# Performance work log

Measured on AMD Instinct MI355X. Metric: run time of the kernel, lower is better.

Reference implementation:

```python
import jax, jax.numpy as jnp
import numpy as np

B, L, D, E, R, NMOD = 8, 2048, 4096, 4, 8, 7

def setup_inputs() -> dict:
    key = jax.random.key(0)
    ks = jax.random.split(key, 8)
    return {
        "x": jax.random.normal(ks[0], (B, L, D), dtype=jnp.float32) * 0.02,
        "expert_scores": jax.random.uniform(ks[1], (B, E), dtype=jnp.float32),
        "W_base": jax.random.normal(ks[2], (D, D), dtype=jnp.float32) * 0.02,
        "b_base": jnp.zeros((D,), dtype=jnp.float32),
        "gating_W": jax.random.normal(ks[3], (D, D), dtype=jnp.float32) * 0.02,
        "W_r": jax.random.normal(ks[4], (NMOD, D), dtype=jnp.float32) * 0.02,
        "lora_A": jax.random.normal(ks[5], (E, R, D), dtype=jnp.float32) * 0.02,
        "lora_B": jax.random.normal(ks[6], (E, D, R), dtype=jnp.float32) * 0.02,
        "module_idx": 0,
        "k": 2,
    }

def _gate_weights(expert_scores, module_prob, k, dtype):
    # rank experts by their random score (descending); Top-K -> weight 1/K
    order = jnp.argsort(-expert_scores, axis=-1)           # [B, E]
    rank = jnp.argsort(order, axis=-1)                     # [B, E] rank of each expert
    k_lo = max(1, k // 2)
    w_hi = (rank < k).astype(dtype) / k                    # prob > 0.5 branch
    w_lo = (rank < k_lo).astype(dtype) / k_lo              # prob <= 0.5 branch
    return jnp.where((module_prob > 0.5)[:, None], w_hi, w_lo)  # [B, E]

def reference(x, expert_scores, W_base, b_base, gating_W, W_r, lora_A, lora_B, module_idx, k):
    # Pooler: last token representation
    pooled = x[:, -1, :]                                   # [B, D]
    # Router: softmax(g(h) W_r) -> per-module probability
    gated = pooled @ gating_W.T                            # [B, D]
    logits = gated @ W_r.T                                 # [B, NMOD]
    probs = jax.nn.softmax(logits, axis=-1)
    module_prob = probs[:, module_idx]                     # [B]
    gate = _gate_weights(expert_scores, module_prob, k, x.dtype)  # [B, E]
    # Base linear projection
    base = x @ W_base.T + b_base                           # [B, L, D]
    # LoRA experts: sum_e gate[b,e] * (x @ A_e^T) @ B_e^T
    t = jnp.einsum('bli,eri->belr', x, lora_A)             # [B, E, L, R]
    lora = jnp.einsum('belr,eor,be->blo', t, lora_B, gate) # [B, L, D]
    return base + lora
```

## Files before the change

kernel.cpp:

```cpp
#include <hip/hip_runtime.h>
#include <hip/hip_bf16.h>


typedef short short8 __attribute__((ext_vector_type(8)));
typedef float f32x4v __attribute__((ext_vector_type(4)));

#define M_DIM 16384
#define N_DIM 4096
#define K_DIM 4160
#define D_DIM 4096
#define NGRP 130

__device__ __forceinline__ unsigned short f2b(float f) {
  unsigned u = __builtin_bit_cast(unsigned, f);
  return (unsigned short)((u + 0x7FFFu + ((u >> 16) & 1u)) >> 16);
}
__device__ __forceinline__ void async_copy16(void* lds, const void* g) {
  __builtin_amdgcn_global_load_lds(
      (const __attribute__((address_space(1))) void*)g,
      (__attribute__((address_space(3))) void*)lds, 16, 0, 0);
}
__device__ __forceinline__ short8 frag_ld(const short* base, int row, int ks, int hi, int lo) {
  return *(const short8*)(&base[row * 64 + (((ks * 4 + hi) ^ (lo & 7)) * 8)]);
}

__global__ __launch_bounds__(256) void cvt_x_k(const float* __restrict__ x,
                                               short* __restrict__ xa) {
  size_t idx = (size_t)blockIdx.x * 256 + threadIdx.x;
  size_t row = idx / 520;
  int cc = (int)(idx % 520);
  short8 o;
  if (cc < 512) {
    const float* src = x + row * (size_t)D_DIM + (size_t)cc * 8;
    float4 a = *(const float4*)(src);
    float4 b = *(const float4*)(src + 4);
    o[0] = (short)f2b(a.x); o[1] = (short)f2b(a.y);
    o[2] = (short)f2b(a.z); o[3] = (short)f2b(a.w);
    o[4] = (short)f2b(b.x); o[5] = (short)f2b(b.y);
    o[6] = (short)f2b(b.z); o[7] = (short)f2b(b.w);
  } else {
#pragma unroll
    for (int t = 0; t < 8; ++t) o[t] = 0;
  }
  *(short8*)(xa + row * (size_t)K_DIM + (size_t)cc * 8) = o;
}

__global__ __launch_bounds__(256) void cvt_w_la_k(const float* __restrict__ Wb,
                                                  const float* __restrict__ lB,
                                                  const float* __restrict__ lA,
                                                  short* __restrict__ wa,
                                                  short* __restrict__ lAb) {
  if (blockIdx.x < 8320) {
    size_t idx = (size_t)blockIdx.x * 256 + threadIdx.x;
    size_t row = idx / 520;
    int cc = (int)(idx % 520);
    short8 o;
    if (cc < 512) {
      const float* src = Wb + row * (size_t)D_DIM + (size_t)cc * 8;
      float4 a = *(const float4*)(src);
      float4 b = *(const float4*)(src + 4);
      o[0] = (short)f2b(a.x); o[1] = (short)f2b(a.y);
      o[2] = (short)f2b(a.z); o[3] = (short)f2b(a.w);
      o[4] = (short)f2b(b.x); o[5] = (short)f2b(b.y);
      o[6] = (short)f2b(b.z); o[7] = (short)f2b(b.w);
    } else if (cc < 516) {
      int e = cc - 512;
      const float* src = lB + (size_t)e * (D_DIM * 8) + row * 8;
      float4 a = *(const float4*)(src);
      float4 b = *(const float4*)(src + 4);
      o[0] = (short)f2b(a.x); o[1] = (short)f2b(a.y);
      o[2] = (short)f2b(a.z); o[3] = (short)f2b(a.w);
      o[4] = (short)f2b(b.x); o[5] = (short)f2b(b.y);
      o[6] = (short)f2b(b.z); o[7] = (short)f2b(b.w);
    } else {
#pragma unroll
      for (int t = 0; t < 8; ++t) o[t] = 0;
    }
    *(short8*)(wa + row * (size_t)K_DIM + (size_t)cc * 8) = o;
  } else {
    size_t i = (size_t)(blockIdx.x - 8320) * 256 + threadIdx.x;
    const float* s = lA + i * 8;
    float4 a = *(const float4*)s;
    float4 b = *(const float4*)(s + 4);
    short8 o;
    o[0] = (short)f2b(a.x); o[1] = (short)f2b(a.y);
    o[2] = (short)f2b(a.z); o[3] = (short)f2b(a.w);
    o[4] = (short)f2b(b.x); o[5] = (short)f2b(b.y);
    o[6] = (short)f2b(b.z); o[7] = (short)f2b(b.w);
    *(short8*)(lAb + i * 8) = o;
  }
}

__global__ __launch_bounds__(256) void gated_k(const float* __restrict__ x,
                                               const float* __restrict__ gW,
                                               float* __restrict__ gated) {
  const int j = blockIdx.x;
  const int tid = threadIdx.x;
  float acc[8];
#pragma unroll
  for (int b = 0; b < 8; ++b) acc[b] = 0.f;
  const float* w = gW + (size_t)j * D_DIM;
  for (int i = tid * 4; i < D_DIM; i += 1024) {
    float4 wv = *(const float4*)(w + i);
#pragma unroll
    for (int b = 0; b < 8; ++b) {
      const float* p = x + ((size_t)b * 2048 + 2047) * D_DIM + i;
      float4 pv = *(const float4*)p;
      acc[b] += wv.x * pv.x + wv.y * pv.y + wv.z * pv.z + wv.w * pv.w;
    }
  }
  __shared__ float red[8][4];
  const int lane = tid & 63, wv_ = tid >> 6;
#pragma unroll
  for (int b = 0; b < 8; ++b) {
    float v = acc[b];
    v += __shfl_down(v, 32); v += __shfl_down(v, 16); v += __shfl_down(v, 8);
    v += __shfl_down(v, 4);  v += __shfl_down(v, 2);  v += __shfl_down(v, 1);
    if (lane == 0) red[b][wv_] = v;
  }
  __syncthreads();
  if (tid < 8)
    gated[(size_t)tid * D_DIM + j] = red[tid][0] + red[tid][1] + red[tid][2] + red[tid][3];
}

__global__ void gate_k(const float* __restrict__ gated, const float* __restrict__ Wr,
                       const float* __restrict__ scores, const int* __restrict__ midx_p,
                       const int* __restrict__ kp, float* __restrict__ gate) {
  const int lane = threadIdx.x;
  float acc[56];
#pragma unroll
  for (int t = 0; t < 56; ++t) acc[t] = 0.f;
  for (int i = lane * 4; i < D_DIM; i += 256) {
    float4 g[8]; float4 w[7];
#pragma unroll
    for (int b = 0; b < 8; ++b) g[b] = *(const float4*)(gated + (size_t)b * D_DIM + i);
#pragma unroll
    for (int m = 0; m < 7; ++m) w[m] = *(const float4*)(Wr + (size_t)m * D_DIM + i);
#pragma unroll
    for (int m = 0; m < 7; ++m)
#pragma unroll
      for (int b = 0; b < 8; ++b)
        acc[m * 8 + b] += w[m].x * g[b].x + w[m].y * g[b].y + w[m].z * g[b].z + w[m].w * g[b].w;
  }
  __shared__ float Ls[56];
#pragma unroll
  for (int t = 0; t < 56; ++t) {
    float v = acc[t];
    v += __shfl_xor(v, 1); v += __shfl_xor(v, 2); v += __shfl_xor(v, 4);
    v += __shfl_xor(v, 8); v += __shfl_xor(v, 16); v += __shfl_xor(v, 32);
    if (lane == t) Ls[t] = v;
  }
  __syncthreads();
  if (lane < 8) {
    const int b = lane;
    float mx = -1e30f;
    for (int m = 0; m < 7; ++m) mx = fmaxf(mx, Ls[m * 8 + b]);
    float s = 0.f;
    for (int m = 0; m < 7; ++m) s += expf(Ls[m * 8 + b] - mx);
    const int mi = midx_p[0];
    const float mp = expf(Ls[mi * 8 + b] - mx) / s;
    int kv = kp[0]; if (kv < 1) kv = 1;
    int klo = kv >> 1; if (klo < 1) klo = 1;
    float sc[4];
#pragma unroll
    for (int e = 0; e < 4; ++e) sc[e] = scores[b * 4 + e];
#pragma unroll
    for (int e = 0; e < 4; ++e) {
      int rank = 0;
#pragma unroll
      for (int e2 = 0; e2 < 4; ++e2)
        rank += (sc[e2] > sc[e] || (sc[e2] == sc[e] && e2 < e)) ? 1 : 0;
      float wv = (mp > 0.5f) ? ((rank < kv) ? 1.0f / (float)kv : 0.f)
                             : ((rank < klo) ? 1.0f / (float)klo : 0.f);
      gate[b * 4 + e] = wv;
    }
  }
}

__global__ __launch_bounds__(256) void lora_t_k(const short* __restrict__ XA,
                                                const short* __restrict__ LAb,
                                                const float* __restrict__ gate,
                                                short* __restrict__ xa_w) {
  __shared__ short As[4096];
  __shared__ short Bs[2048];
  const int tid = threadIdx.x, lane = tid & 63, wave = tid >> 6;
  const int lo = lane & 15, hi = lane >> 4;
  const size_t row0 = (size_t)blockIdx.x * 64;
  const int srow = tid >> 3;
  const int slot = (tid & 7) ^ (srow & 7);
  const short* gA = XA + (row0 + srow) * (size_t)K_DIM + slot * 8;
  const short* gB = LAb + (size_t)srow * D_DIM + slot * 8;
  f32x4v acc[2] = {};

  for (int t = 0; t < 64; ++t) {
    const int kt = t * 64;
    char* la = (char*)As + wave * 1024;
    char* lb = (char*)Bs + wave * 1024;
    async_copy16(la, gA + kt);
    async_copy16(la + 4096, gA + (size_t)32 * K_DIM + kt);
    async_copy16(lb, gB + kt);
    __syncthreads();
    short8 a0 = frag_ld(As, wave * 16 + lo, 0, hi, lo);
    short8 a1 = frag_ld(As, wave * 16 + lo, 1, hi, lo);
    short8 b00 = frag_ld(Bs, lo, 0, hi, lo);
    short8 b01 = frag_ld(Bs, lo, 1, hi, lo);
    short8 b10 = frag_ld(Bs, 16 + lo, 0, hi, lo);
    short8 b11 = frag_ld(Bs, 16 + lo, 1, hi, lo);
    acc[0] = __builtin_amdgcn_mfma_f32_16x16x32_bf16(a0, b00, acc[0], 0, 0, 0);
    acc[0] = __builtin_amdgcn_mfma_f32_16x16x32_bf16(a1, b01, acc[0], 0, 0, 0);
    acc[1] = __builtin_amdgcn_mfma_f32_16x16x32_bf16(a0, b10, acc[1], 0, 0, 0);
    acc[1] = __builtin_amdgcn_mfma_f32_16x16x32_bf16(a1, b11, acc[1], 0, 0, 0);
    __syncthreads();
  }
  const int b = (int)(row0 >> 11);
#pragma unroll
  for (int ni = 0; ni < 2; ++ni) {
    const int col = ni * 16 + lo;
    const float g = gate[b * 4 + (col >> 3)];
#pragma unroll
    for (int j = 0; j < 4; ++j) {
      const size_t r = row0 + wave * 16 + hi * 4 + j;
      xa_w[r * (size_t)K_DIM + 4096 + col] = (short)f2b(acc[ni][j] * g);
    }
  }
}

__global__ __launch_bounds__(512, 2) void gemm_k(const short* __restrict__ A,
                                                 const short* __restrict__ B,
                                                 const float* __restrict__ bias,
                                                 float* __restrict__ C) {
  __shared__ short As[5][8192];
  __shared__ short Bs[5][8192];
  const int tid = threadIdx.x;
  const int lane = tid & 63;
  const int wave = tid >> 6;
  const int wm = wave >> 2;
  const int wn = wave & 3;
  const int lo = lane & 15, hi = lane >> 4;

  const int wg = (blockIdx.x & 7) * 128 + (blockIdx.x >> 3);
  const int brow = wg >> 4;
  const int bcol = wg & 15;

  const int srow = tid >> 2;
  const int schunk = (tid & 3) ^ ((tid >> 3) & 3);
  const short* srcA = A + (size_t)(brow * 256 + srow) * K_DIM + schunk * 8;
  const short* srcB = B + (size_t)(bcol * 256 + srow) * K_DIM + schunk * 8;
  char* ldsA0 = (char*)(&As[0][0]) + wave * 1024;
  char* ldsB0 = (char*)(&Bs[0][0]) + wave * 1024;

  const int csw = (hi ^ ((lo >> 1) & 3)) * 8;
  const int aro = (wm * 128 + lo) * 32 + csw;
  const int bro = (wn * 64 + lo) * 32 + csw;

  float bz[4];
#pragma unroll
  for (int ni = 0; ni < 4; ++ni)
    bz[ni] = bias[bcol * 256 + wn * 64 + ni * 16 + lo];

  f32x4v acc[8][4] = {};

#define STAGE_A(koff, ss)                                                      \
  async_copy16(ldsA0 + (ss) * 16384, srcA + (koff));                           \
  async_copy16(ldsA0 + (ss) * 16384 + 8192, srcA + (size_t)128 * K_DIM + (koff));
#define STAGE_B(koff, ss)                                                      \
  async_copy16(ldsB0 + (ss) * 16384, srcB + (koff));                           \
  async_copy16(ldsB0 + (ss) * 16384 + 8192, srcB + (size_t)128 * K_DIM + (koff));

#define GROUP(s, ko, sw)                                                       \
  {                                                                            \
    const short* Aslot = &As[0][0] + (s) * 8192;                               \
    const short* Bslot = &Bs[0][0] + (s) * 8192;                               \
    short8 afr[4], afr2[4], bfr[4];                                            \
    _Pragma("unroll")                                                          \
    for (int mi = 0; mi < 4; ++mi)                                             \
      afr[mi] = *(const short8*)(&Aslot[aro + mi * 512]);                      \
    _Pragma("unroll")                                                          \
    for (int ni = 0; ni < 4; ++ni)                                             \
      bfr[ni] = *(const short8*)(&Bslot[bro + ni * 512]);                      \
    _Pragma("unroll")                                                          \
    for (int mi = 0; mi < 4; ++mi)                                             \
      afr2[mi] = *(const short8*)(&Aslot[aro + 2048 + mi * 512]);              \
    __builtin_amdgcn_s_setprio(1);                                             \
    _Pragma("unroll")                                                          \
    for (int mi = 0; mi < 4; ++mi)                                             \
      _Pragma("unroll")                                                        \
      for (int ni = 0; ni < 4; ++ni)                                           \
        acc[mi][ni] = __builtin_amdgcn_mfma_f32_16x16x32_bf16(                 \
            afr[mi], bfr[ni], acc[mi][ni], 0, 0, 0);                           \
    __builtin_amdgcn_s_setprio(0);                                             \
    STAGE_A((ko), (sw));                                                       \
    STAGE_B((ko), (sw));                                                       \
    __builtin_amdgcn_s_setprio(1);                                             \
    _Pragma("unroll")                                                          \
    for (int mi = 0; mi < 4; ++mi)                                             \
      _Pragma("unroll")                                                        \
      for (int ni = 0; ni < 4; ++ni)                                           \
        acc[mi + 4][ni] = __builtin_amdgcn_mfma_f32_16x16x32_bf16(             \
            afr2[mi], bfr[ni], acc[mi + 4][ni], 0, 0, 0);                      \
    __builtin_amdgcn_s_setprio(0);                                             \
  }

  STAGE_A(0, 0);  STAGE_B(0, 0);
  STAGE_A(32, 1); STAGE_B(32, 1);
  STAGE_A(64, 2); STAGE_B(64, 2);
  asm volatile("s_waitcnt vmcnt(4)" ::: "memory");
  __builtin_amdgcn_s_barrier();

  int s0 = 0;
  for (int p = 0; p < 65; ++p) {
    const int g0 = 2 * p, g1 = g0 + 1;
    const int s1  = (s0 + 1 == 5) ? 0 : s0 + 1;
    const int sw0 = (s0 + 3 >= 5) ? s0 - 2 : s0 + 3;
    const int sw1 = (sw0 + 1 == 5) ? 0 : sw0 + 1;
    const size_t ko0 = (size_t)((g0 + 3 <= NGRP - 1) ? g0 + 3 : g0 - 2) * 32;
    const size_t ko1 = (size_t)((g1 + 3 <= NGRP - 1) ? g1 + 3 : g1 - 2) * 32;

    GROUP(s0, ko0, sw0)
    GROUP(s1, ko1, sw1)

    asm volatile("s_waitcnt vmcnt(4)" ::: "memory");
    __builtin_amdgcn_s_barrier();
    s0 = (s0 + 2 >= 5) ? s0 - 3 : s0 + 2;
  }
  asm volatile("s_waitcnt vmcnt(0)" ::: "memory");

#pragma unroll
  for (int mi = 0; mi < 8; ++mi) {
#pragma unroll
    for (int ni = 0; ni < 4; ++ni) {
      const int r0 = brow * 256 + wm * 128 + mi * 16 + hi * 4;
      const int c0 = bcol * 256 + wn * 64 + ni * 16 + lo;
#pragma unroll
      for (int j = 0; j < 4; ++j)
        C[(size_t)(r0 + j) * N_DIM + c0] = acc[mi][ni][j] + bz[ni];
    }
  }
#undef GROUP
#undef STAGE_A
#undef STAGE_B
}

extern "C" void kernel_launch(void* const* d_in, const int* in_sizes, int n_in,
                              void* d_out, int out_size, void* d_ws, size_t ws_size,
                              hipStream_t stream) {
  const float* x      = (const float*)d_in[0];
  const float* scores = (const float*)d_in[1];
  const float* Wb     = (const float*)d_in[2];
  const float* bb     = (const float*)d_in[3];
  const float* gW     = (const float*)d_in[4];
  const float* Wr     = (const float*)d_in[5];
  const float* lA     = (const float*)d_in[6];
  const float* lB     = (const float*)d_in[7];
  const int*   midx   = (const int*)d_in[8];
  const int*   kk     = (const int*)d_in[9];
  float* out = (float*)d_out;

  char* ws = (char*)d_ws;
  short* xa    = (short*)ws;
  short* wa    = (short*)(ws + 136314880u);
  float* gated = (float*)(ws + 136314880u + 34078720u);
  float* gate  = (float*)(ws + 136314880u + 34078720u + 131072u);
  short* lAb   = (short*)(ws + 136314880u + 34078720u + 131072u + 128u);

  cvt_x_k<<<33280, 256, 0, stream>>>(x, xa);
  cvt_w_la_k<<<8384, 256, 0, stream>>>(Wb, lB, lA, wa, lAb);
  gated_k<<<4096, 256, 0, stream>>>(x, gW, gated);
  gate_k<<<1, 64, 0, stream>>>(gated, Wr, scores, midx, kk, gate);
  lora_t_k<<<256, 256, 0, stream>>>(xa, lAb, gate, xa);
  gemm_k<<<1024, 512, 0, stream>>>(xa, wa, bb, out);
}
```

Baseline: 703.4 us.

## Pipeline LoRA-A projection kernel with 4-stage async loads and smaller row tiles

```diff
diff --git a/kernel.cpp b/kernel.cpp
--- a/kernel.cpp
+++ b/kernel.cpp
@@ -181,48 +181,55 @@
                                                 const short* __restrict__ LAb,
                                                 const float* __restrict__ gate,
                                                 short* __restrict__ xa_w) {
-  __shared__ short As[4096];
-  __shared__ short Bs[2048];
+  __shared__ short As[4][2048];
+  __shared__ short Bs[4][2048];
   const int tid = threadIdx.x, lane = tid & 63, wave = tid >> 6;
   const int lo = lane & 15, hi = lane >> 4;
-  const size_t row0 = (size_t)blockIdx.x * 64;
+  const int wr = (wave >> 1) * 16;
+  const int wc = (wave & 1) * 16;
+  const size_t row0 = (size_t)blockIdx.x * 32;
   const int srow = tid >> 3;
-  const int slot = (tid & 7) ^ (srow & 7);
-  const short* gA = XA + (row0 + srow) * (size_t)K_DIM + slot * 8;
-  const short* gB = LAb + (size_t)srow * D_DIM + slot * 8;
-  f32x4v acc[2] = {};
-
-  for (int t = 0; t < 64; ++t) {
-    const int kt = t * 64;
-    char* la = (char*)As + wave * 1024;
-    char* lb = (char*)Bs + wave * 1024;
-    async_copy16(la, gA + kt);
-    async_copy16(la + 4096, gA + (size_t)32 * K_DIM + kt);
-    async_copy16(lb, gB + kt);
-    __syncthreads();
-    short8 a0 = frag_ld(As, wave * 16 + lo, 0, hi, lo);
-    short8 a1 = frag_ld(As, wave * 16 + lo, 1, hi, lo);
-    short8 b00 = frag_ld(Bs, lo, 0, hi, lo);
-    short8 b01 = frag_ld(Bs, lo, 1, hi, lo);
-    short8 b10 = frag_ld(Bs, 16 + lo, 0, hi, lo);
-    short8 b11 = frag_ld(Bs, 16 + lo, 1, hi, lo);
-    acc[0] = __builtin_amdgcn_mfma_f32_16x16x32_bf16(a0, b00, acc[0], 0, 0, 0);
-    acc[0] = __builtin_amdgcn_mfma_f32_16x16x32_bf16(a1, b01, acc[0], 0, 0, 0);
-    acc[1] = __builtin_amdgcn_mfma_f32_16x16x32_bf16(a0, b10, acc[1], 0, 0, 0);
-    acc[1] = __builtin_amdgcn_mfma_f32_16x16x32_bf16(a1, b11, acc[1], 0, 0, 0);
-    __syncthreads();
-  }
+  const int sslot = (tid & 7) ^ (srow & 7);
+  const short* gA = XA + (row0 + srow) * (size_t)K_DIM + sslot * 8;
+  const short* gB = LAb + (size_t)srow * D_DIM + sslot * 8;
+  f32x4v acc = {};
+
+#define LSTAGE(g)                                                              \
+  async_copy16((char*)&As[(g) & 3][0] + wave * 1024, gA + (size_t)(g) * 64);   \
+  async_copy16((char*)&Bs[(g) & 3][0] + wave * 1024, gB + (size_t)(g) * 64);
+
+  LSTAGE(0)
+  LSTAGE(1)
+  asm volatile("s_waitcnt vmcnt(2)" ::: "memory");
+  __builtin_amdgcn_s_barrier();
+
+  for (int g = 0; g < 64; ++g) {
+    const short* Atile = &As[g & 3][0];
+    const short* Btile = &Bs[g & 3][0];
+    short8 a0 = frag_ld(Atile, wr + lo, 0, hi, lo);
+    short8 a1 = frag_ld(Atile, wr + lo, 1, hi, lo);
+    short8 b0 = frag_ld(Btile, wc + lo, 0, hi, lo);
+    short8 b1 = frag_ld(Btile, wc + lo, 1, hi, lo);
+    acc = __builtin_amdgcn_mfma_f32_16x16x32_bf16(a0, b0, acc, 0, 0, 0);
+    acc = __builtin_amdgcn_mfma_f32_16x16x32_bf16(a1, b1, acc, 0, 0, 0);
+    if (g < 62) {
+      LSTAGE(g + 2)
+      asm volatile("s_waitcnt vmcnt(2)" ::: "memory");
+    } else {
+      asm volatile("s_waitcnt vmcnt(0)" ::: "memory");
+    }
+    __builtin_amdgcn_s_barrier();
+  }
+
   const int b = (int)(row0 >> 11);
-#pragma unroll
-  for (int ni = 0; ni < 2; ++ni) {
-    const int col = ni * 16 + lo;
-    const float g = gate[b * 4 + (col >> 3)];
-#pragma unroll
-    for (int j = 0; j < 4; ++j) {
-      const size_t r = row0 + wave * 16 + hi * 4 + j;
-      xa_w[r * (size_t)K_DIM + 4096 + col] = (short)f2b(acc[ni][j] * g);
-    }
-  }
+  const int col = wc + lo;
+  const float gv = gate[b * 4 + (col >> 3)];
+#pragma unroll
+  for (int j = 0; j < 4; ++j) {
+    const size_t r = row0 + wr + hi * 4 + j;
+    xa_w[r * (size_t)K_DIM + 4096 + col] = (short)f2b(acc[j] * gv);
+  }
+#undef LSTAGE
 }
 
 __global__ __launch_bounds__(512, 2) void gemm_k(const short* __restrict__ A,
@@ -367,6 +374,6 @@
   cvt_w_la_k<<<8384, 256, 0, stream>>>(Wb, lB, lA, wa, lAb);
   gated_k<<<4096, 256, 0, stream>>>(x, gW, gated);
   gate_k<<<1, 64, 0, stream>>>(gated, Wr, scores, midx, kk, gate);
-  lora_t_k<<<256, 256, 0, stream>>>(xa, lAb, gate, xa);
+  lora_t_k<<<512, 256, 0, stream>>>(xa, lAb, gate, xa);
   gemm_k<<<1024, 512, 0, stream>>>(xa, wa, bb, out);
 }
```

Result: no change. 696.4 us (-1.0%).
